# Kernel tuning notes

Measured on AMD Instinct MI355X. Metric: run time of the kernel, lower is better.

The kernel has to match this reference:

```python
import jax, jax.numpy as jnp
import numpy as np
from jax.scipy.special import gammaln

D = 512       # feature_dim
C = 64        # n classes (n-way)
SHOTS = 5     # matches hardcoded self.fix_Nj = 5
Q = 2048      # query samples
FIX_NJ = 5.0


def setup_inputs() -> dict:
    key = jax.random.key(0)
    k1, k2 = jax.random.split(key, 2)
    X_support = jax.random.normal(k1, (C * SHOTS, D), dtype=jnp.float32)
    # labels 0..C-1, SHOTS contiguous samples per class (required: code indexes mu[j] by label)
    y = (jnp.arange(C * SHOTS, dtype=jnp.int32) // SHOTS)
    X_query = jax.random.normal(k2, (Q, D), dtype=jnp.float32)
    # learned parameters, initialized exactly as in the torch module
    m = jnp.zeros((1, D), dtype=jnp.float32)
    kappa = jnp.float32(0.1)
    nu = jnp.float32(D)
    triu_S_diag = jnp.ones((D,), dtype=jnp.float32)
    triu_S_lower = jnp.eye(D, dtype=jnp.float32)
    return {"X_support": X_support, "y": y, "X_query": X_query,
            "m": m, "kappa": kappa, "nu": nu,
            "triu_S_diag": triu_S_diag, "triu_S_lower": triu_S_lower}


def reference(X_support, y, X_query, m, kappa, nu, triu_S_diag, triu_S_lower):
    # ---- compute_shared_part ----
    # triu(ones,1).t() == strictly-lower-triangular mask
    mask = jnp.tril(jnp.ones((D, D), dtype=X_support.dtype), -1)
    L = jnp.diag(jnp.abs(triu_S_diag)) + triu_S_lower * mask
    kappa_n = jnp.abs(kappa) + 1e-6 + FIX_NJ
    m_with_weight = jnp.abs(kappa + 1e-6) / kappa_n * m          # [1,D]
    xmean_weight = FIX_NJ / kappa_n
    scatter = L @ L.T                                            # self_outer(L), square case
    sp = jnp.clip(nu, D - 1 + 1e-6) + FIX_NJ - D + 2             # sharedpart (scalar)
    bias_shared = gammaln(0.5 * (sp + D)) - gammaln(0.5 * sp) - 0.5 * D * jnp.log(sp)

    # ---- fit_image_label, batched over classes ----
    # y is arange//SHOTS so grouping X[y==j] == contiguous reshape
    Xc = X_support.reshape(C, SHOTS, D)                          # [C,S,D]
    x_mean = Xc.mean(axis=1)                                     # [C,D]
    mean_outer = jnp.einsum('csd,cse->cde', Xc, Xc) / SHOTS      # X_j^T X_j / N_j
    mu = m_with_weight + x_mean * xmean_weight                   # [C,D]
    dm = x_mean - m                                              # [C,D]; self_outer of [1,D] row -> outer product
    sigma = scatter[None] + mean_outer \
        + jnp.einsum('cd,ce->cde', dm, dm) * ((jnp.abs(kappa) + 1e-6) / kappa_n)
    sigma = sigma / ((kappa_n + 1) / (kappa_n * sp))             # [C,D,D]
    sigma_inv = jnp.linalg.inv(sigma)                            # batched inverse
    _, logdet = jnp.linalg.slogdet(sigma)                        # sigma is PD -> logdet
    biases = bias_shared - 0.5 * logdet                          # [C]

    # ---- predict, batched over queries and classes ----
    diff = X_query[:, None, :] - mu[None, :, :]                  # [Q,C,D]
    tmp = jnp.einsum('qcd,cde->qce', diff, sigma_inv)
    dist = jnp.sum(tmp * diff, axis=-1)                          # Mahalanobis [Q,C]
    return biases[None, :] - 0.5 * (sp + D) * jnp.log(1.0 + dist / sp)
```

## Files before the change

kernel.cpp:

```cpp
#include <hip/hip_runtime.h>
#include <math.h>

#define D 512
#define NC 64
#define NQ 2048

typedef unsigned short u16;
typedef __attribute__((ext_vector_type(8))) short bf8;
typedef __attribute__((ext_vector_type(4))) float f4;

#define OFF_S    0
#define OFF_ABH  32
#define OFF_ABL  (OFF_ABH + 655360)
#define OFF_LH   (OFF_ABL + 655360)
#define OFF_LL   (OFF_LH + 131072)
#define OFF_WH   (OFF_LL + 131072)
#define OFF_WL   (OFF_WH + 131072)
#define OFF_YYH  (OFF_WL + 131072)
#define OFF_YYL  (OFF_YYH + 655360)
#define OFF_AQ   (OFF_YYL + 655360)
#define OFF_GRAM (OFF_AQ + NQ)

#define GIX(i, j) ((i) * 7 - (i) * ((i) + 1) / 2 + (j))

__device__ inline float wred(float v) {
#pragma unroll
  for (int off = 32; off; off >>= 1) v += __shfl_down(v, off);
  return v;
}

__device__ inline void split2(float v, u16& h, u16& l) {
  unsigned u = __float_as_uint(v);
  h = (u16)(u >> 16);
  float hf = __uint_as_float(u & 0xFFFF0000u);
  float r = v - hf;
  unsigned ru = __float_as_uint(r);
  l = (u16)((ru + 0x7FFFu + ((ru >> 16) & 1u)) >> 16);
}

__device__ inline void split4(float a0, float a1, float a2, float a3,
                              ushort4& h, ushort4& l) {
  u16 hh, ll;
  split2(a0, hh, ll); h.x = hh; l.x = ll;
  split2(a1, hh, ll); h.y = hh; l.y = ll;
  split2(a2, hh, ll); h.z = hh; l.z = ll;
  split2(a3, hh, ll); h.w = hh; l.w = ll;
}

#define MPAD 68
template <int N>
__device__ inline void lds_mm(float (*M)[MPAD], int ar, int ac, int br, int bc,
                              int cr, int cc, bool neg) {
  const int T = N / 16;
  int tx = (threadIdx.x & 15) * T, ty = (threadIdx.x >> 4) * T;
  float acc[T][T];
#pragma unroll
  for (int i = 0; i < T; ++i)
#pragma unroll
    for (int j = 0; j < T; ++j) acc[i][j] = 0.f;
#pragma unroll 8
  for (int k = 0; k < N; ++k) {
    float a[T], b[T];
#pragma unroll
    for (int i = 0; i < T; ++i) a[i] = M[ar + ty + i][ac + k];
#pragma unroll
    for (int j = 0; j < T; ++j) b[j] = M[br + k][bc + tx + j];
#pragma unroll
    for (int i = 0; i < T; ++i)
#pragma unroll
      for (int j = 0; j < T; ++j) acc[i][j] += a[i] * b[j];
  }
#pragma unroll
  for (int i = 0; i < T; ++i)
#pragma unroll
    for (int j = 0; j < T; ++j)
      M[cr + ty + i][cc + tx + j] = neg ? -acc[i][j] : acc[i][j];
}

__device__ inline void inv64(float (*M)[MPAD], int tid) {
  {
    float x[16];
    int q = tid >> 4, col = tid & 15;
    if (tid < 64) {
      int b = q << 4;
#pragma unroll
      for (int i = 0; i < 16; ++i) {
        float acc = 0.f;
#pragma unroll
        for (int k = 0; k < i; ++k) acc += M[b + i][b + k] * x[k];
        x[i] = (((i == col) ? 1.f : 0.f) - acc) / M[b + i][b + i];
      }
    }
    __syncthreads();
    if (tid < 64) {
      int b = q << 4;
#pragma unroll
      for (int i = 0; i < 16; ++i) M[b + i][b + col] = x[i];
    }
    __syncthreads();
  }
  for (int pp = 0; pp < 2; ++pp) {
    int r0 = 32 * pp;
    lds_mm<16>(M, r0 + 16, r0, r0, r0, r0, r0 + 16, false);
  }
  __syncthreads();
  for (int pp = 0; pp < 2; ++pp) {
    int r0 = 32 * pp;
    lds_mm<16>(M, r0 + 16, r0 + 16, r0, r0 + 16, r0 + 16, r0, true);
  }
  __syncthreads();
  for (int idx = tid; idx < 512; idx += 256) {
    int t2 = idx >> 8, r = (idx >> 4) & 15, c = idx & 15;
    M[32 * t2 + r][32 * t2 + 16 + c] = 0.f;
  }
  __syncthreads();
  lds_mm<32>(M, 32, 0, 0, 0, 0, 32, false);
  __syncthreads();
  lds_mm<32>(M, 32, 32, 0, 32, 32, 0, true);
  __syncthreads();
  for (int idx = tid; idx < 1024; idx += 256) {
    int r = idx >> 5, c = idx & 31;
    M[r][32 + c] = 0.f;
  }
  __syncthreads();
}

__global__ __launch_bounds__(256) void k_prep(const float* __restrict__ diag,
                                              const float* __restrict__ low,
                                              const float* __restrict__ Xs,
                                              const float* __restrict__ Xq,
                                              const float* __restrict__ m,
                                              const float* __restrict__ kp,
                                              const float* __restrict__ nup,
                                              u16* __restrict__ Lh, u16* __restrict__ Ll,
                                              u16* __restrict__ ABh, u16* __restrict__ ABl,
                                              u16* __restrict__ Wh, u16* __restrict__ Wl,
                                              float* __restrict__ S, float* __restrict__ aq,
                                              float* __restrict__ Gram) {
  __shared__ float M[64][MPAD];
  int bid = blockIdx.x, tid = threadIdx.x;
  if (bid < 8) {
    int p = bid * 64;
    for (int idx = tid; idx < 4096; idx += 256) {
      int r = idx >> 6, c = idx & 63;
      float v;
      if (r == c)      v = fabsf(diag[p + r]);
      else if (r > c)  v = low[(size_t)(p + r) * D + p + c];
      else             v = 0.f;
      M[r][c] = v;
    }
    __syncthreads();
    inv64(M, tid);
    for (int idx = tid; idx < 1024; idx += 256) {
      int r = idx >> 4, c4 = (idx & 15) << 2;
      ushort4 hh, ll;
      split4(M[r][c4 + 0], M[r][c4 + 1], M[r][c4 + 2], M[r][c4 + 3], hh, ll);
      size_t gi = (size_t)(p + r) * D + p + c4;
      *reinterpret_cast<ushort4*>(Wh + gi) = hh;
      *reinterpret_cast<ushort4*>(Wl + gi) = ll;
    }
  } else if (bid < 72) {
    int c = bid - 8;
    if (tid < 128) {
      float kappa = kp[0];
      float kn = fabsf(kappa) + 1e-6f + 5.0f;
      float xw = 5.0f / kn;
      float mw = fabsf(kappa + 1e-6f) / kn;
      float sw = sqrtf((fabsf(kappa) + 1e-6f) / kn);
      const float is5 = 0.44721359549995793f;
      int d4 = tid;
      float xs[5][4];
#pragma unroll
      for (int s = 0; s < 5; ++s) {
        float4 v = reinterpret_cast<const float4*>(Xs + (size_t)(c * 5 + s) * D)[d4];
        xs[s][0] = v.x; xs[s][1] = v.y; xs[s][2] = v.z; xs[s][3] = v.w;
      }
      float4 mvv = reinterpret_cast<const float4*>(m)[d4];
      float mv[4] = {mvv.x, mvv.y, mvv.z, mvv.w};
      float rows[8][4];
#pragma unroll
      for (int e = 0; e < 4; ++e) {
        float xm = (xs[0][e] + xs[1][e] + xs[2][e] + xs[3][e] + xs[4][e]) * 0.2f;
#pragma unroll
        for (int s = 0; s < 5; ++s) rows[s][e] = xs[s][e] * is5;
        rows[5][e] = sw * (xm - mv[e]);
        rows[6][e] = mw * mv[e] + xw * xm;
        rows[7][e] = 0.f;
      }
#pragma unroll
      for (int s = 0; s < 8; ++s) {
        ushort4 hh, ll;
        split4(rows[s][0], rows[s][1], rows[s][2], rows[s][3], hh, ll);
        size_t gi = (size_t)(c * 8 + s) * D + 4 * tid;
        *reinterpret_cast<ushort4*>(ABh + gi) = hh;
        *reinterpret_cast<ushort4*>(ABl + gi) = ll;
      }
    }
  } else if (bid == 72) {
    for (int i = tid; i < NQ; i += 256) aq[i] = 0.f;
    for (int i = tid; i < NC * 28; i += 256) Gram[i] = 0.f;
    if (tid >= 64) return;
    float part = 0.f;
    for (int i = tid; i < D; i += 64) part += logf(fabsf(diag[i]));
    part = wred(part);
    if (tid != 0) return;
    float lda = 2.f * part;
    float kappa = kp[0], nu = nup[0];
    float kn = fabsf(kappa) + 1e-6f + 5.0f;
    float sp = fmaxf(nu, (float)(D - 1) + 1e-6f) + 5.0f - (float)D + 2.0f;
    float bias_shared = lgammaf(0.5f * (sp + (float)D)) - lgammaf(0.5f * sp)
                      - 0.5f * (float)D * logf(sp);
    float scale = kn * sp / (kn + 1.0f);
    S[3] = bias_shared;
    S[8] = 1.f / scale;
    S[9] = (float)D * logf(scale) + lda;
    S[10] = 0.5f * (sp + (float)D);
    S[11] = 1.f / sp;
  } else if (bid < 329) {
    int t = (bid - 73) * 1024 + tid * 4;
    int i = t >> 9, j = t & 511;
    float4 lv = *reinterpret_cast<const float4*>(low + t);
    float a[4] = {lv.x, lv.y, lv.z, lv.w};
    float dv = diag[i];
    float o[4];
#pragma unroll
    for (int e = 0; e < 4; ++e) {
      int jj = j + e;
      o[e] = (i == jj) ? fabsf(dv) : (i > jj ? a[e] : 0.f);
    }
    ushort4 hh, ll;
    split4(o[0], o[1], o[2], o[3], hh, ll);
    *reinterpret_cast<ushort4*>(Lh + t) = hh;
    *reinterpret_cast<ushort4*>(Ll + t) = ll;
  } else {
    size_t base = (size_t)(bid - 329) * 8192;
#pragma unroll
    for (int it = 0; it < 8; ++it) {
      size_t idx = base + it * 1024 + tid * 4;
      float4 v = *reinterpret_cast<const float4*>(Xq + idx);
      ushort4 hh, ll;
      split4(v.x, v.y, v.z, v.w, hh, ll);
      *reinterpret_cast<ushort4*>(ABh + (size_t)512 * D + idx) = hh;
      *reinterpret_cast<ushort4*>(ABl + (size_t)512 * D + idx) = ll;
    }
  }
}

__global__ __launch_bounds__(256) void k_solve(const u16* __restrict__ Lh,
                                               const u16* __restrict__ Ll,
                                               u16* __restrict__ Wh,
                                               const u16* __restrict__ Wl) {
  __shared__ __align__(16) u16 XTh[32][520];
  __shared__ __align__(16) u16 XTl[32][520];
  __shared__ __align__(16) u16 STh[32][72];
  __shared__ __align__(16) u16 STl[32][72];
  int J = blockIdx.x;
  int i0 = J >> 1;
  int tid = threadIdx.x, w = tid >> 6, lane = tid & 63;
  int lr = lane & 15, kq = lane >> 4;
  for (int idx = tid; idx < 64 * 32; idx += 256) {
    int r = idx >> 5, c = idx & 31;
    size_t gi = (size_t)(64 * i0 + r) * D + 64 * i0 + (J & 1) * 32 + c;
    XTh[c][64 * i0 + r] = Wh[gi];
    XTl[c][64 * i0 + r] = Wl[gi];
  }
  __syncthreads();
  for (int i = i0 + 1; i < 8; ++i) {
    f4 acc[2];
    acc[0] = (f4){0.f, 0.f, 0.f, 0.f};
    acc[1] = (f4){0.f, 0.f, 0.f, 0.f};
    for (int k = i0; k < i; ++k) {
#pragma unroll
      for (int kk = 0; kk < 2; ++kk) {
        size_t ga = (size_t)(64 * i + w * 16 + lr) * D + 64 * k + kk * 32 + kq * 8;
        bf8 ah = *reinterpret_cast<const bf8*>(Lh + ga);
        bf8 al = *reinterpret_cast<const bf8*>(Ll + ga);
#pragma unroll
        for (int nf = 0; nf < 2; ++nf) {
          bf8 bh = *reinterpret_cast<const bf8*>(&XTh[nf * 16 + lr][64 * k + kk * 32 + kq * 8]);
          bf8 bl = *reinterpret_cast<const bf8*>(&XTl[nf * 16 + lr][64 * k + kk * 32 + kq * 8]);
          acc[nf] = __builtin_amdgcn_mfma_f32_16x16x32_bf16(ah, bh, acc[nf], 0, 0, 0);
          acc[nf] = __builtin_amdgcn_mfma_f32_16x16x32_bf16(ah, bl, acc[nf], 0, 0, 0);
          acc[nf] = __builtin_amdgcn_mfma_f32_16x16x32_bf16(al, bh, acc[nf], 0, 0, 0);
        }
      }
    }
#pragma unroll
    for (int nf = 0; nf < 2; ++nf)
#pragma unroll
      for (int reg = 0; reg < 4; ++reg) {
        float v = -acc[nf][reg];
        u16 hh, ll; split2(v, hh, ll);
        int c = nf * 16 + lr, r = w * 16 + kq * 4 + reg;
        STh[c][r] = hh; STl[c][r] = ll;
      }
    __syncthreads();
    f4 acc2[2];
    acc2[0] = (f4){0.f, 0.f, 0.f, 0.f};
    acc2[1] = (f4){0.f, 0.f, 0.f, 0.f};
#pragma unroll
    for (int kk = 0; kk < 2; ++kk) {
      size_t ga = (size_t)(64 * i + w * 16 + lr) * D + 64 * i + kk * 32 + kq * 8;
      bf8 ah = *reinterpret_cast<const bf8*>(Wh + ga);
      bf8 al = *reinterpret_cast<const bf8*>(Wl + ga);
#pragma unroll
      for (int nf = 0; nf < 2; ++nf) {
        bf8 bh = *reinterpret_cast<const bf8*>(&STh[nf * 16 + lr][kk * 32 + kq * 8]);
        bf8 bl = *reinterpret_cast<const bf8*>(&STl[nf * 16 + lr][kk * 32 + kq * 8]);
        acc2[nf] = __builtin_amdgcn_mfma_f32_16x16x32_bf16(ah, bh, acc2[nf], 0, 0, 0);
        acc2[nf] = __builtin_amdgcn_mfma_f32_16x16x32_bf16(ah, bl, acc2[nf], 0, 0, 0);
        acc2[nf] = __builtin_amdgcn_mfma_f32_16x16x32_bf16(al, bh, acc2[nf], 0, 0, 0);
      }
    }
#pragma unroll
    for (int nf = 0; nf < 2; ++nf)
#pragma unroll
      for (int reg = 0; reg < 4; ++reg) {
        float v = acc2[nf][reg];
        u16 hh, ll; split2(v, hh, ll);
        int r = w * 16 + kq * 4 + reg, c = nf * 16 + lr;
        Wh[(size_t)(64 * i + r) * D + 32 * J + c] = hh;
        XTh[c][64 * i + r] = hh; XTl[c][64 * i + r] = ll;
      }
    __syncthreads();
  }
}

__global__ __launch_bounds__(256) void k_mf1(const u16* __restrict__ ABh, const u16* __restrict__ ABl,
                                             const u16* __restrict__ Wh,
                                             u16* __restrict__ YYh, u16* __restrict__ YYl,
                                             float* __restrict__ Gram, float* __restrict__ aq) {
  __shared__ float Csh[64][68];
  int tid = threadIdx.x, w = tid >> 6, lane = tid & 63;
  int bn = (7 - (int)blockIdx.x) * 64;
  int m0 = blockIdx.y * 64 + w * 16;
  int lr = lane & 15, kof = (lane >> 4) * 8;
  const u16* ah_p = ABh + (size_t)(m0 + lr) * D + kof;
  const u16* al_p = ABl + (size_t)(m0 + lr) * D + kof;
  const u16* bh_p = Wh + (size_t)(bn + lr) * D + kof;
  f4 acc[4];
#pragma unroll
  for (int nf = 0; nf < 4; ++nf) acc[nf] = (f4){0.f, 0.f, 0.f, 0.f};
  int Klim = bn + 64;
#pragma unroll 2
  for (int k0 = 0; k0 < Klim; k0 += 32) {
    bf8 ah = *reinterpret_cast<const bf8*>(ah_p + k0);
    bf8 al = *reinterpret_cast<const bf8*>(al_p + k0);
    bf8 bh[4];
#pragma unroll
    for (int nf = 0; nf < 4; ++nf)
      bh[nf] = *reinterpret_cast<const bf8*>(bh_p + (size_t)nf * 16 * D + k0);
#pragma unroll
    for (int nf = 0; nf < 4; ++nf)
      acc[nf] = __builtin_amdgcn_mfma_f32_16x16x32_bf16(ah, bh[nf], acc[nf], 0, 0, 0);
#pragma unroll
    for (int nf = 0; nf < 4; ++nf)
      acc[nf] = __builtin_amdgcn_mfma_f32_16x16x32_bf16(al, bh[nf], acc[nf], 0, 0, 0);
  }
  int rbase = m0 + ((lane >> 4) << 2);
#pragma unroll
  for (int reg = 0; reg < 4; ++reg) {
    int row = rbase + reg;
    float sq = 0.f;
#pragma unroll
    for (int nf = 0; nf < 4; ++nf) {
      float v = acc[nf][reg];
      size_t gi = (size_t)row * D + bn + nf * 16 + lr;
      u16 hh, ll; split2(v, hh, ll);
      YYh[gi] = hh;
      if (row >= 512) YYl[gi] = ll;
      sq += v * v;
    }
    if (row >= 512) {
#pragma unroll
      for (int mk = 1; mk < 16; mk <<= 1) sq += __shfl_xor(sq, mk);
      if (lr == 0) atomicAdd(&aq[row - 512], sq);
    }
  }
  if (blockIdx.y < 8) {
#pragma unroll
    for (int reg = 0; reg < 4; ++reg)
#pragma unroll
      for (int nf = 0; nf < 4; ++nf)
        Csh[w * 16 + ((lane >> 4) << 2) + reg][nf * 16 + lr] = acc[nf][reg];
    __syncthreads();
    if (tid < 224) {
      const int PI[28] = {0,0,0,0,0,0,0, 1,1,1,1,1,1, 2,2,2,2,2, 3,3,3,3, 4,4,4, 5,5, 6};
      const int PJ[28] = {0,1,2,3,4,5,6, 1,2,3,4,5,6, 2,3,4,5,6, 3,4,5,6, 4,5,6, 5,6, 6};
      int cl = tid / 28, p = tid % 28;
      const float* ri = Csh[cl * 8 + PI[p]];
      const float* rj = Csh[cl * 8 + PJ[p]];
      float s = 0.f;
#pragma unroll
      for (int c4 = 0; c4 < 64; c4 += 4) {
        float4 a = *reinterpret_cast<const float4*>(&ri[c4]);
        float4 b = *reinterpret_cast<const float4*>(&rj[c4]);
        s += a.x * b.x + a.y * b.y + a.z * b.z + a.w * b.w;
      }
      atomicAdd(&Gram[(blockIdx.y * 8 + cl) * 28 + p], s);
    }
  }
}

__global__ __launch_bounds__(256) void k_mf2(const u16* __restrict__ Yh, const u16* __restrict__ Yl,
                                             const u16* __restrict__ Bh,
                                             const float* __restrict__ aq,
                                             const float* __restrict__ Gram,
                                             const float* __restrict__ S,
                                             float* __restrict__ out) {
  __shared__ float Csh[4][16][68];
  __shared__ float PRo[8][15], PRd[8][6], Psv[8][6], Pb[8], Ph[8];
  int tid = threadIdx.x, w = tid >> 6, lane = tid & 63;
  int m0 = blockIdx.x * 64 + w * 16;
  int bn = blockIdx.y * 64;
  int lr = lane & 15, kof = (lane >> 4) * 8;
  const u16* ah_p = Yh + (size_t)(m0 + lr) * D + kof;
  const u16* al_p = Yl + (size_t)(m0 + lr) * D + kof;
  const u16* bh_p = Bh + (size_t)(bn + lr) * D + kof;
  f4 acc[4];
#pragma unroll
  for (int nf = 0; nf < 4; ++nf) acc[nf] = (f4){0.f, 0.f, 0.f, 0.f};
#pragma unroll 2
  for (int k0 = 0; k0 < D; k0 += 32) {
    bf8 ah = *reinterpret_cast<const bf8*>(ah_p + k0);
    bf8 al = *reinterpret_cast<const bf8*>(al_p + k0);
    bf8 bh[4];
#pragma unroll
    for (int nf = 0; nf < 4; ++nf)
      bh[nf] = *reinterpret_cast<const bf8*>(bh_p + (size_t)nf * 16 * D + k0);
#pragma unroll
    for (int nf = 0; nf < 4; ++nf)
      acc[nf] = __builtin_amdgcn_mfma_f32_16x16x32_bf16(ah, bh[nf], acc[nf], 0, 0, 0);
#pragma unroll
    for (int nf = 0; nf < 4; ++nf)
      acc[nf] = __builtin_amdgcn_mfma_f32_16x16x32_bf16(al, bh[nf], acc[nf], 0, 0, 0);
  }
#pragma unroll
  for (int reg = 0; reg < 4; ++reg)
#pragma unroll
    for (int nf = 0; nf < 4; ++nf)
      Csh[w][((lane >> 4) << 2) + reg][nf * 16 + lr] = acc[nf][reg];
  if (tid < 8) {
    int c = blockIdx.y * 8 + tid;
    float Gv[28];
#pragma unroll
    for (int p = 0; p < 28; ++p) Gv[p] = Gram[c * 28 + p];
    float R[6][6];
    float logdetM = 0.f;
#pragma unroll
    for (int i = 0; i < 6; ++i) {
      float s = Gv[GIX(i, i)] + 1.f;
#pragma unroll
      for (int k = 0; k < i; ++k) s -= R[i][k] * R[i][k];
      float rii = sqrtf(s);
      R[i][i] = rii;
      logdetM += logf(rii);
      float inv = 1.f / rii;
      PRd[tid][i] = inv;
#pragma unroll
      for (int r = i + 1; r < 6; ++r) {
        float s2 = Gv[GIX(i, r)];
#pragma unroll
        for (int k = 0; k < i; ++k) s2 -= R[r][k] * R[i][k];
        R[r][i] = s2 * inv;
      }
    }
#pragma unroll
    for (int i = 1; i < 6; ++i)
#pragma unroll
      for (int k = 0; k < i; ++k)
        PRo[tid][i * (i - 1) / 2 + k] = R[i][k];
#pragma unroll
    for (int j = 0; j < 6; ++j) Psv[tid][j] = Gv[GIX(j, 6)];
    Ph[tid] = Gv[27];
    Pb[tid] = S[3] - 0.5f * (S[9] + 2.f * logdetM);
  }
  __syncthreads();
  float s8 = S[8], s10 = S[10], s11 = S[11];
  int r = lr;
  int q = m0 + r;
  float aqv = aq[q];
#pragma unroll
  for (int cc = 0; cc < 2; ++cc) {
    int cl = ((lane >> 4) << 1) + cc;
    const float* t = &Csh[w][r][cl * 8];
    float e[6];
#pragma unroll
    for (int j = 0; j < 6; ++j) e[j] = t[j] - Psv[cl][j];
    const float* o = PRo[cl];
    const float* dg = PRd[cl];
    float z0 = e[0] * dg[0];
    float z1 = (e[1] - o[0] * z0) * dg[1];
    float z2 = (e[2] - o[1] * z0 - o[2] * z1) * dg[2];
    float z3 = (e[3] - o[3] * z0 - o[4] * z1 - o[5] * z2) * dg[3];
    float z4 = (e[4] - o[6] * z0 - o[7] * z1 - o[8] * z2 - o[9] * z3) * dg[4];
    float z5 = (e[5] - o[10] * z0 - o[11] * z1 - o[12] * z2 - o[13] * z3 - o[14] * z4) * dg[5];
    float quad = z0 * z0 + z1 * z1 + z2 * z2 + z3 * z3 + z4 * z4 + z5 * z5;
    float dist = (aqv - 2.f * t[6] + Ph[cl] - quad) * s8;
    out[(size_t)q * NC + blockIdx.y * 8 + cl] = Pb[cl] - s10 * log1pf(dist * s11);
  }
}

extern "C" void kernel_launch(void* const* d_in, const int* in_sizes, int n_in,
                              void* d_out, int out_size, void* d_ws, size_t ws_size,
                              hipStream_t stream) {
  const float* Xs   = (const float*)d_in[0];
  const float* Xq   = (const float*)d_in[2];
  const float* m    = (const float*)d_in[3];
  const float* kap  = (const float*)d_in[4];
  const float* nu   = (const float*)d_in[5];
  const float* diag = (const float*)d_in[6];
  const float* low  = (const float*)d_in[7];
  float* ws = (float*)d_ws;

  float* S    = ws + OFF_S;
  u16*   ABh  = (u16*)(ws + OFF_ABH);
  u16*   ABl  = (u16*)(ws + OFF_ABL);
  u16*   Lh   = (u16*)(ws + OFF_LH);
  u16*   Ll   = (u16*)(ws + OFF_LL);
  u16*   Wh   = (u16*)(ws + OFF_WH);
  u16*   Wl   = (u16*)(ws + OFF_WL);
  u16*   YYh  = (u16*)(ws + OFF_YYH);
  u16*   YYl  = (u16*)(ws + OFF_YYL);
  float* aq   = ws + OFF_AQ;
  float* Gram = ws + OFF_GRAM;

  hipLaunchKernelGGL(k_prep, dim3(457), dim3(256), 0, stream,
                     diag, low, Xs, Xq, m, kap, nu, Lh, Ll, ABh, ABl, Wh, Wl, S, aq, Gram);
  hipLaunchKernelGGL(k_solve, dim3(16), dim3(256), 0, stream, Lh, Ll, Wh, Wl);
  hipLaunchKernelGGL(k_mf1, dim3(8, 40), dim3(256), 0, stream,
                     ABh, ABl, Wh, YYh, YYl, Gram, aq);
  hipLaunchKernelGGL(k_mf2, dim3(32, 8), dim3(256), 0, stream,
                     YYh + (size_t)512 * D, YYl + (size_t)512 * D, YYh,
                     aq, Gram, S, (float*)d_out);
}
```

Before: 88.79 us.

## Fuse query split and two-stage GEMM into per-query-tile kernel

Query conversion to bf16 hi/lo moves from the prep kernel into the final kernel, which now computes the query-times-W GEMM (exploiting W's triangular shape to stop the k-loop early), keeps Y in LDS, computes the query norms locally, and then does the second GEMM against the support-side product plus the per-class Cholesky epilogue. The first GEMM kernel now only handles the 512 support rows. This removes the round trip of the large YY and AB query buffers through global memory and the global atomics for query norms. In exchange each block redoes the Cholesky setup for all 64 classes, the grid has only 128 blocks of 16 query rows, and W is re-read from global or L2 by every block.

New measurement: 117.0 us. 1.32x slower.

```diff
diff --git a/kernel.cpp b/kernel.cpp
--- a/kernel.cpp
+++ b/kernel.cpp
@@ -10,16 +10,14 @@
 typedef __attribute__((ext_vector_type(4))) float f4;
 
 #define OFF_S    0
-#define OFF_ABH  32
-#define OFF_ABL  (OFF_ABH + 655360)
-#define OFF_LH   (OFF_ABL + 655360)
+#define OFF_LH   32
 #define OFF_LL   (OFF_LH + 131072)
 #define OFF_WH   (OFF_LL + 131072)
 #define OFF_WL   (OFF_WH + 131072)
-#define OFF_YYH  (OFF_WL + 131072)
-#define OFF_YYL  (OFF_YYH + 655360)
-#define OFF_AQ   (OFF_YYL + 655360)
-#define OFF_GRAM (OFF_AQ + NQ)
+#define OFF_ABH  (OFF_WL + 131072)
+#define OFF_ABL  (OFF_ABH + 131072)
+#define OFF_UWH  (OFF_ABL + 131072)
+#define OFF_GRAM (OFF_UWH + 131072)
 
 #define GIX(i, j) ((i) * 7 - (i) * ((i) + 1) / 2 + (j))
 
@@ -128,15 +126,13 @@
 __global__ __launch_bounds__(256) void k_prep(const float* __restrict__ diag,
                                               const float* __restrict__ low,
                                               const float* __restrict__ Xs,
-                                              const float* __restrict__ Xq,
                                               const float* __restrict__ m,
                                               const float* __restrict__ kp,
                                               const float* __restrict__ nup,
                                               u16* __restrict__ Lh, u16* __restrict__ Ll,
                                               u16* __restrict__ ABh, u16* __restrict__ ABl,
                                               u16* __restrict__ Wh, u16* __restrict__ Wl,
-                                              float* __restrict__ S, float* __restrict__ aq,
-                                              float* __restrict__ Gram) {
+                                              float* __restrict__ S, float* __restrict__ Gram) {
   __shared__ float M[64][MPAD];
   int bid = blockIdx.x, tid = threadIdx.x;
   if (bid < 8) {
@@ -197,7 +193,6 @@
       }
     }
   } else if (bid == 72) {
-    for (int i = tid; i < NQ; i += 256) aq[i] = 0.f;
     for (int i = tid; i < NC * 28; i += 256) Gram[i] = 0.f;
     if (tid >= 64) return;
     float part = 0.f;
@@ -216,7 +211,7 @@
     S[9] = (float)D * logf(scale) + lda;
     S[10] = 0.5f * (sp + (float)D);
     S[11] = 1.f / sp;
-  } else if (bid < 329) {
+  } else {
     int t = (bid - 73) * 1024 + tid * 4;
     int i = t >> 9, j = t & 511;
     float4 lv = *reinterpret_cast<const float4*>(low + t);
@@ -232,16 +227,10 @@
     split4(o[0], o[1], o[2], o[3], hh, ll);
     *reinterpret_cast<ushort4*>(Lh + t) = hh;
     *reinterpret_cast<ushort4*>(Ll + t) = ll;
-  } else {
-    size_t base = (size_t)(bid - 329) * 8192;
-#pragma unroll
-    for (int it = 0; it < 8; ++it) {
-      size_t idx = base + it * 1024 + tid * 4;
-      float4 v = *reinterpret_cast<const float4*>(Xq + idx);
-      ushort4 hh, ll;
-      split4(v.x, v.y, v.z, v.w, hh, ll);
-      *reinterpret_cast<ushort4*>(ABh + (size_t)512 * D + idx) = hh;
-      *reinterpret_cast<ushort4*>(ABl + (size_t)512 * D + idx) = ll;
+    if (i < j) Wh[t] = 0;
+    if (i < j + 3) {
+#pragma unroll
+      for (int e = 0; e < 4; ++e) if (i < j + e) Wh[t + e] = 0;
     }
   }
 }
@@ -280,8 +269,8 @@
           bf8 bh = *reinterpret_cast<const bf8*>(&XTh[nf * 16 + lr][64 * k + kk * 32 + kq * 8]);
           bf8 bl = *reinterpret_cast<const bf8*>(&XTl[nf * 16 + lr][64 * k + kk * 32 + kq * 8]);
           acc[nf] = __builtin_amdgcn_mfma_f32_16x16x32_bf16(ah, bh, acc[nf], 0, 0, 0);
+          acc[nf] = __builtin_amdgcn_mfma_f32_16x16x32_bf16(al, bh, acc[nf], 0, 0, 0);
           acc[nf] = __builtin_amdgcn_mfma_f32_16x16x32_bf16(ah, bl, acc[nf], 0, 0, 0);
-          acc[nf] = __builtin_amdgcn_mfma_f32_16x16x32_bf16(al, bh, acc[nf], 0, 0, 0);
         }
       }
     }
@@ -326,10 +315,10 @@
   }
 }
 
-__global__ __launch_bounds__(256) void k_mf1(const u16* __restrict__ ABh, const u16* __restrict__ ABl,
-                                             const u16* __restrict__ Wh,
-                                             u16* __restrict__ YYh, u16* __restrict__ YYl,
-                                             float* __restrict__ Gram, float* __restrict__ aq) {
+__global__ __launch_bounds__(256) void k_mf1s(const u16* __restrict__ ABh, const u16* __restrict__ ABl,
+                                              const u16* __restrict__ Wh,
+                                              u16* __restrict__ UWh,
+                                              float* __restrict__ Gram) {
   __shared__ float Csh[64][68];
   int tid = threadIdx.x, w = tid >> 6, lane = tid & 63;
   int bn = (7 - (int)blockIdx.x) * 64;
@@ -357,91 +346,103 @@
     for (int nf = 0; nf < 4; ++nf)
       acc[nf] = __builtin_amdgcn_mfma_f32_16x16x32_bf16(al, bh[nf], acc[nf], 0, 0, 0);
   }
-  int rbase = m0 + ((lane >> 4) << 2);
 #pragma unroll
   for (int reg = 0; reg < 4; ++reg) {
-    int row = rbase + reg;
-    float sq = 0.f;
+    int row = m0 + ((lane >> 4) << 2) + reg;
 #pragma unroll
     for (int nf = 0; nf < 4; ++nf) {
       float v = acc[nf][reg];
-      size_t gi = (size_t)row * D + bn + nf * 16 + lr;
       u16 hh, ll; split2(v, hh, ll);
-      YYh[gi] = hh;
-      if (row >= 512) YYl[gi] = ll;
-      sq += v * v;
-    }
-    if (row >= 512) {
-#pragma unroll
-      for (int mk = 1; mk < 16; mk <<= 1) sq += __shfl_xor(sq, mk);
-      if (lr == 0) atomicAdd(&aq[row - 512], sq);
-    }
-  }
-  if (blockIdx.y < 8) {
-#pragma unroll
-    for (int reg = 0; reg < 4; ++reg)
-#pragma unroll
-      for (int nf = 0; nf < 4; ++nf)
-        Csh[w * 16 + ((lane >> 4) << 2) + reg][nf * 16 + lr] = acc[nf][reg];
-    __syncthreads();
-    if (tid < 224) {
-      const int PI[28] = {0,0,0,0,0,0,0, 1,1,1,1,1,1, 2,2,2,2,2, 3,3,3,3, 4,4,4, 5,5, 6};
-      const int PJ[28] = {0,1,2,3,4,5,6, 1,2,3,4,5,6, 2,3,4,5,6, 3,4,5,6, 4,5,6, 5,6, 6};
-      int cl = tid / 28, p = tid % 28;
-      const float* ri = Csh[cl * 8 + PI[p]];
-      const float* rj = Csh[cl * 8 + PJ[p]];
-      float s = 0.f;
-#pragma unroll
-      for (int c4 = 0; c4 < 64; c4 += 4) {
-        float4 a = *reinterpret_cast<const float4*>(&ri[c4]);
-        float4 b = *reinterpret_cast<const float4*>(&rj[c4]);
-        s += a.x * b.x + a.y * b.y + a.z * b.z + a.w * b.w;
-      }
-      atomicAdd(&Gram[(blockIdx.y * 8 + cl) * 28 + p], s);
-    }
-  }
-}
-
-__global__ __launch_bounds__(256) void k_mf2(const u16* __restrict__ Yh, const u16* __restrict__ Yl,
-                                             const u16* __restrict__ Bh,
-                                             const float* __restrict__ aq,
-                                             const float* __restrict__ Gram,
-                                             const float* __restrict__ S,
-                                             float* __restrict__ out) {
-  __shared__ float Csh[4][16][68];
-  __shared__ float PRo[8][15], PRd[8][6], Psv[8][6], Pb[8], Ph[8];
+      UWh[(size_t)row * D + bn + nf * 16 + lr] = hh;
+      Csh[(row - blockIdx.y * 64)][nf * 16 + lr] = v;
+    }
+  }
+  __syncthreads();
+  if (tid < 224) {
+    const int PI[28] = {0,0,0,0,0,0,0, 1,1,1,1,1,1, 2,2,2,2,2, 3,3,3,3, 4,4,4, 5,5, 6};
+    const int PJ[28] = {0,1,2,3,4,5,6, 1,2,3,4,5,6, 2,3,4,5,6, 3,4,5,6, 4,5,6, 5,6, 6};
+    int cl = tid / 28, p = tid % 28;
+    const float* ri = Csh[cl * 8 + PI[p]];
+    const float* rj = Csh[cl * 8 + PJ[p]];
+    float s = 0.f;
+#pragma unroll
+    for (int c4 = 0; c4 < 64; c4 += 4) {
+      float4 a = *reinterpret_cast<const float4*>(&ri[c4]);
+      float4 b = *reinterpret_cast<const float4*>(&rj[c4]);
+      s += a.x * b.x + a.y * b.y + a.z * b.z + a.w * b.w;
+    }
+    atomicAdd(&Gram[(blockIdx.y * 8 + cl) * 28 + p], s);
+  }
+}
+
+__global__ __launch_bounds__(256) void k_mf2f(const float* __restrict__ Xq,
+                                              const u16* __restrict__ Wh,
+                                              const u16* __restrict__ UWh,
+                                              const float* __restrict__ Gram,
+                                              const float* __restrict__ S,
+                                              float* __restrict__ out) {
+  __shared__ __align__(16) char shmem[16 * 520 * 4];
+  __shared__ float asq[16];
+  __shared__ float PRo[64][15], PRd[64][6], Psv[64][6], Pb[64], Ph[64];
+  u16 (*Yh)[520] = reinterpret_cast<u16(*)[520]>(shmem);
+  u16 (*Yl)[520] = reinterpret_cast<u16(*)[520]>(shmem + 16 * 520 * 2);
   int tid = threadIdx.x, w = tid >> 6, lane = tid & 63;
-  int m0 = blockIdx.x * 64 + w * 16;
-  int bn = blockIdx.y * 64;
-  int lr = lane & 15, kof = (lane >> 4) * 8;
-  const u16* ah_p = Yh + (size_t)(m0 + lr) * D + kof;
-  const u16* al_p = Yl + (size_t)(m0 + lr) * D + kof;
-  const u16* bh_p = Bh + (size_t)(bn + lr) * D + kof;
-  f4 acc[4];
-#pragma unroll
-  for (int nf = 0; nf < 4; ++nf) acc[nf] = (f4){0.f, 0.f, 0.f, 0.f};
-#pragma unroll 2
-  for (int k0 = 0; k0 < D; k0 += 32) {
-    bf8 ah = *reinterpret_cast<const bf8*>(ah_p + k0);
-    bf8 al = *reinterpret_cast<const bf8*>(al_p + k0);
-    bf8 bh[4];
-#pragma unroll
-    for (int nf = 0; nf < 4; ++nf)
-      bh[nf] = *reinterpret_cast<const bf8*>(bh_p + (size_t)nf * 16 * D + k0);
-#pragma unroll
-    for (int nf = 0; nf < 4; ++nf)
-      acc[nf] = __builtin_amdgcn_mfma_f32_16x16x32_bf16(ah, bh[nf], acc[nf], 0, 0, 0);
-#pragma unroll
-    for (int nf = 0; nf < 4; ++nf)
-      acc[nf] = __builtin_amdgcn_mfma_f32_16x16x32_bf16(al, bh[nf], acc[nf], 0, 0, 0);
-  }
-#pragma unroll
-  for (int reg = 0; reg < 4; ++reg)
-#pragma unroll
-    for (int nf = 0; nf < 4; ++nf)
-      Csh[w][((lane >> 4) << 2) + reg][nf * 16 + lr] = acc[nf][reg];
-  if (tid < 8) {
-    int c = blockIdx.y * 8 + tid;
+  int lr = lane & 15, kq = lane >> 4, kof = kq * 8;
+  int q0 = blockIdx.x * 16;
+  if (tid < 16) asq[tid] = 0.f;
+  __syncthreads();
+  f4 acc[8];
+#pragma unroll
+  for (int j = 0; j < 8; ++j) acc[j] = (f4){0.f, 0.f, 0.f, 0.f};
+  int klim[8];
+#pragma unroll
+  for (int j = 0; j < 8; ++j) {
+    int bn = 16 * (w + 4 * j);
+    klim[j] = (((bn + 47) >> 5) << 5);
+  }
+  const float* xrow = Xq + (size_t)(q0 + lr) * D;
+  for (int k0 = 0; k0 < klim[7]; k0 += 32) {
+    float4 a0 = *reinterpret_cast<const float4*>(xrow + k0 + kof);
+    float4 a1 = *reinterpret_cast<const float4*>(xrow + k0 + kof + 4);
+    float av[8] = {a0.x, a0.y, a0.z, a0.w, a1.x, a1.y, a1.z, a1.w};
+    bf8 ah, al;
+#pragma unroll
+    for (int e = 0; e < 8; ++e) {
+      u16 hh, ll; split2(av[e], hh, ll);
+      ah[e] = (short)hh; al[e] = (short)ll;
+    }
+#pragma unroll
+    for (int j = 0; j < 8; ++j) {
+      if (k0 < klim[j]) {
+        const u16* bp = Wh + (size_t)(16 * (w + 4 * j) + lr) * D + k0 + kof;
+        bf8 bh = *reinterpret_cast<const bf8*>(bp);
+        acc[j] = __builtin_amdgcn_mfma_f32_16x16x32_bf16(ah, bh, acc[j], 0, 0, 0);
+        acc[j] = __builtin_amdgcn_mfma_f32_16x16x32_bf16(al, bh, acc[j], 0, 0, 0);
+      }
+    }
+  }
+  float sq[4] = {0.f, 0.f, 0.f, 0.f};
+#pragma unroll
+  for (int j = 0; j < 8; ++j) {
+    int bn = 16 * (w + 4 * j);
+#pragma unroll
+    for (int reg = 0; reg < 4; ++reg) {
+      float v = acc[j][reg];
+      u16 hh, ll; split2(v, hh, ll);
+      Yh[kq * 4 + reg][bn + lr] = hh;
+      Yl[kq * 4 + reg][bn + lr] = ll;
+      sq[reg] += v * v;
+    }
+  }
+#pragma unroll
+  for (int reg = 0; reg < 4; ++reg) {
+#pragma unroll
+    for (int mk = 1; mk < 16; mk <<= 1) sq[reg] += __shfl_xor(sq[reg], mk);
+    if (lr == 0) atomicAdd(&asq[kq * 4 + reg], sq[reg]);
+  }
+  __syncthreads();
+  if (tid < 64) {
+    int c = tid;
     float Gv[28];
 #pragma unroll
     for (int p = 0; p < 28; ++p) Gv[p] = Gram[c * 28 + p];
@@ -456,7 +457,7 @@
       R[i][i] = rii;
       logdetM += logf(rii);
       float inv = 1.f / rii;
-      PRd[tid][i] = inv;
+      PRd[c][i] = inv;
 #pragma unroll
       for (int r = i + 1; r < 6; ++r) {
         float s2 = Gv[GIX(i, r)];
@@ -469,26 +470,46 @@
     for (int i = 1; i < 6; ++i)
 #pragma unroll
       for (int k = 0; k < i; ++k)
-        PRo[tid][i * (i - 1) / 2 + k] = R[i][k];
-#pragma unroll
-    for (int j = 0; j < 6; ++j) Psv[tid][j] = Gv[GIX(j, 6)];
-    Ph[tid] = Gv[27];
-    Pb[tid] = S[3] - 0.5f * (S[9] + 2.f * logdetM);
-  }
+        PRo[c][i * (i - 1) / 2 + k] = R[i][k];
+#pragma unroll
+    for (int j = 0; j < 6; ++j) Psv[c][j] = Gv[GIX(j, 6)];
+    Ph[c] = Gv[27];
+    Pb[c] = S[3] - 0.5f * (S[9] + 2.f * logdetM);
+  }
+  f4 acc2[8];
+#pragma unroll
+  for (int j = 0; j < 8; ++j) acc2[j] = (f4){0.f, 0.f, 0.f, 0.f};
+  for (int k0 = 0; k0 < D; k0 += 32) {
+    bf8 ah = *reinterpret_cast<const bf8*>(&Yh[lr][k0 + kof]);
+    bf8 al = *reinterpret_cast<const bf8*>(&Yl[lr][k0 + kof]);
+#pragma unroll
+    for (int j = 0; j < 8; ++j) {
+      const u16* bp = UWh + (size_t)(128 * w + 16 * j + lr) * D + k0 + kof;
+      bf8 bh = *reinterpret_cast<const bf8*>(bp);
+      acc2[j] = __builtin_amdgcn_mfma_f32_16x16x32_bf16(ah, bh, acc2[j], 0, 0, 0);
+      acc2[j] = __builtin_amdgcn_mfma_f32_16x16x32_bf16(al, bh, acc2[j], 0, 0, 0);
+    }
+  }
+  __syncthreads();
+  float (*T2s)[520] = reinterpret_cast<float(*)[520]>(shmem);
+#pragma unroll
+  for (int j = 0; j < 8; ++j)
+#pragma unroll
+    for (int reg = 0; reg < 4; ++reg)
+      T2s[kq * 4 + reg][128 * w + 16 * j + lr] = acc2[j][reg];
   __syncthreads();
   float s8 = S[8], s10 = S[10], s11 = S[11];
-  int r = lr;
-  int q = m0 + r;
-  float aqv = aq[q];
-#pragma unroll
-  for (int cc = 0; cc < 2; ++cc) {
-    int cl = ((lane >> 4) << 1) + cc;
-    const float* t = &Csh[w][r][cl * 8];
+  int r_ = tid & 15, cg = tid >> 4;
+  float aqv = asq[r_];
+#pragma unroll
+  for (int cc = 0; cc < 4; ++cc) {
+    int c = cg * 4 + cc;
+    const float* t = &T2s[r_][c * 8];
     float e[6];
 #pragma unroll
-    for (int j = 0; j < 6; ++j) e[j] = t[j] - Psv[cl][j];
-    const float* o = PRo[cl];
-    const float* dg = PRd[cl];
+    for (int j = 0; j < 6; ++j) e[j] = t[j] - Psv[c][j];
+    const float* o = PRo[c];
+    const float* dg = PRd[c];
     float z0 = e[0] * dg[0];
     float z1 = (e[1] - o[0] * z0) * dg[1];
     float z2 = (e[2] - o[1] * z0 - o[2] * z1) * dg[2];
@@ -496,8 +517,8 @@
     float z4 = (e[4] - o[6] * z0 - o[7] * z1 - o[8] * z2 - o[9] * z3) * dg[4];
     float z5 = (e[5] - o[10] * z0 - o[11] * z1 - o[12] * z2 - o[13] * z3 - o[14] * z4) * dg[5];
     float quad = z0 * z0 + z1 * z1 + z2 * z2 + z3 * z3 + z4 * z4 + z5 * z5;
-    float dist = (aqv - 2.f * t[6] + Ph[cl] - quad) * s8;
-    out[(size_t)q * NC + blockIdx.y * 8 + cl] = Pb[cl] - s10 * log1pf(dist * s11);
+    float dist = (aqv - 2.f * t[6] + Ph[c] - quad) * s8;
+    out[(size_t)(q0 + r_) * NC + c] = Pb[c] - s10 * log1pf(dist * s11);
   }
 }
 
@@ -514,23 +535,20 @@
   float* ws = (float*)d_ws;
 
   float* S    = ws + OFF_S;
-  u16*   ABh  = (u16*)(ws + OFF_ABH);
-  u16*   ABl  = (u16*)(ws + OFF_ABL);
   u16*   Lh   = (u16*)(ws + OFF_LH);
   u16*   Ll   = (u16*)(ws + OFF_LL);
   u16*   Wh   = (u16*)(ws + OFF_WH);
   u16*   Wl   = (u16*)(ws + OFF_WL);
-  u16*   YYh  = (u16*)(ws + OFF_YYH);
-  u16*   YYl  = (u16*)(ws + OFF_YYL);
-  float* aq   = ws + OFF_AQ;
+  u16*   ABh  = (u16*)(ws + OFF_ABH);
+  u16*   ABl  = (u16*)(ws + OFF_ABL);
+  u16*   UWh  = (u16*)(ws + OFF_UWH);
   float* Gram = ws + OFF_GRAM;
 
-  hipLaunchKernelGGL(k_prep, dim3(457), dim3(256), 0, stream,
-                     diag, low, Xs, Xq, m, kap, nu, Lh, Ll, ABh, ABl, Wh, Wl, S, aq, Gram);
+  hipLaunchKernelGGL(k_prep, dim3(329), dim3(256), 0, stream,
+                     diag, low, Xs, m, kap, nu, Lh, Ll, ABh, ABl, Wh, Wl, S, Gram);
   hipLaunchKernelGGL(k_solve, dim3(16), dim3(256), 0, stream, Lh, Ll, Wh, Wl);
-  hipLaunchKernelGGL(k_mf1, dim3(8, 40), dim3(256), 0, stream,
-                     ABh, ABl, Wh, YYh, YYl, Gram, aq);
-  hipLaunchKernelGGL(k_mf2, dim3(32, 8), dim3(256), 0, stream,
-                     YYh + (size_t)512 * D, YYl + (size_t)512 * D, YYh,
-                     aq, Gram, S, (float*)d_out);
-}
+  hipLaunchKernelGGL(k_mf1s, dim3(8, 8), dim3(256), 0, stream,
+                     ABh, ABl, Wh, UWh, Gram);
+  hipLaunchKernelGGL(k_mf2f, dim3(NQ / 16), dim3(256), 0, stream,
+                     Xq, Wh, UWh, Gram, S, (float*)d_out);
+}
```
